# Performance work log

Hardware: AMD Instinct MI355X
Metric: run time of the kernel (lower is better)

Reference implementation:

```python
import jax, jax.numpy as jnp
import numpy as np

B = 16384
INPUT_DIM = 768
DIM = 500
K = 43  # known_types(33) + unknown_types(10)
VAE_DIM = 1024


def setup_inputs() -> dict:
    key = jax.random.key(0)
    ks = jax.random.split(key, 12)
    x = jax.random.normal(ks[0], (B, INPUT_DIM), dtype=jnp.float32)
    known_mask = jax.random.randint(ks[1], (B,), 0, 2) > 0
    labels = jax.random.randint(ks[2], (B,), 0, 33)
    eps = jax.random.normal(ks[3], (B, VAE_DIM), dtype=jnp.float32)
    # encoder MLP (layers_n=1): single Linear(input_dim -> dim)
    W_enc = jax.random.normal(ks[4], (DIM, INPUT_DIM), dtype=jnp.float32) * (1.0 / np.sqrt(INPUT_DIM))
    b_enc = jnp.zeros((DIM,), dtype=jnp.float32)
    # codebook embedding, init U(-1/K, 1/K)
    codebook = jax.random.uniform(ks[5], (K, DIM), dtype=jnp.float32, minval=-1.0 / K, maxval=1.0 / K)
    # vae_encoder MLP (layers_n=2): Linear(input_dim->vae_dim), ReLU, Linear(vae_dim->2*vae_dim)
    W1 = jax.random.normal(ks[6], (VAE_DIM, INPUT_DIM), dtype=jnp.float32) * (1.0 / np.sqrt(INPUT_DIM))
    b1 = jnp.zeros((VAE_DIM,), dtype=jnp.float32)
    W2 = jax.random.normal(ks[7], (2 * VAE_DIM, VAE_DIM), dtype=jnp.float32) * (1.0 / np.sqrt(VAE_DIM))
    b2 = jnp.zeros((2 * VAE_DIM,), dtype=jnp.float32)
    # vae_decoder: Linear(K + vae_dim -> input_dim)
    Wd = jax.random.normal(ks[8], (INPUT_DIM, K + VAE_DIM), dtype=jnp.float32) * (1.0 / np.sqrt(K + VAE_DIM))
    bd = jnp.zeros((INPUT_DIM,), dtype=jnp.float32)
    return {
        "x": x, "known_mask": known_mask, "labels": labels, "eps": eps,
        "W_enc": W_enc, "b_enc": b_enc, "codebook": codebook,
        "W1": W1, "b1": b1, "W2": W2, "b2": b2, "Wd": Wd, "bd": bd,
    }


def reference(x, known_mask, labels, eps, W_enc, b_enc, codebook, W1, b1, W2, b2, Wd, bd):
    # encoder: z_e_x (B, dim)
    z_e_x = x @ W_enc.T + b_enc
    # codebook lookup: logits (B, K); argmax of softmax == argmax of logits
    logits = z_e_x @ codebook.T
    y_tilde = jax.nn.softmax(logits, axis=1)
    indices = jnp.argmax(y_tilde, axis=1)
    z_q_x = codebook[indices]  # (B, dim), differentiable gather w.r.t. codebook
    # VAE encoder: mu, logvar (B, vae_dim)
    h = jax.nn.relu(x @ W1.T + b1)
    mu_logvar = h @ W2.T + b2
    mu, logvar = jnp.split(mu_logvar, 2, axis=1)
    # KL( N(mu, exp(0.5*logvar)) || N(0,1) ), summed over dim, mean over batch
    kl_div = jnp.mean(jnp.sum(0.5 * (jnp.exp(logvar) + mu * mu - 1.0 - logvar), axis=1))
    # reparameterized sample
    sampled_z = mu + jnp.exp(0.5 * logvar) * eps
    # replace known rows of y_tilde with one-hot labels
    onehot = jax.nn.one_hot(labels, logits.shape[1], dtype=y_tilde.dtype)
    y = jnp.where(known_mask[:, None], onehot, y_tilde)
    # vae decoder
    x_tilde = jnp.concatenate([sampled_z, y], axis=1) @ Wd.T + bd
    return (x_tilde, z_e_x, z_q_x, logits, kl_div)
```

## Files before the change

kernel.cpp:

```cpp
#include <hip/hip_runtime.h>
#include <hip/hip_bf16.h>
#include <math.h>


#define B_ROWS 16384

typedef __attribute__((ext_vector_type(8))) short bf16x8;
typedef __attribute__((ext_vector_type(4))) float f32x4;

constexpr size_t X_TILDE_OFF = 0;
constexpr size_t ZE_OFF      = 12582912;
constexpr size_t ZQ_OFF      = 20774912;
constexpr size_t LOG_OFF     = 28966912;
constexpr size_t KL_OFF      = 29671424;

constexpr size_t WS_XH  = 0;
constexpr size_t WS_XL  = 25165824;
constexpr size_t WS_ZB  = 50331648;
constexpr size_t WS_HB  = 85983232;
constexpr size_t WS_MLB = 119537664;
constexpr size_t WS_W1B = 186646528;
constexpr size_t WS_W2B = 188219392;
constexpr size_t WS_WDB = 192413696;
constexpr size_t WS_WEH = 194084864;
constexpr size_t WS_WEL = 194871296;
constexpr size_t WS_CBH = 195657728;
constexpr size_t WS_CBL = 195854336;
constexpr size_t WS_CBD = 196050944;
constexpr size_t WS_LBF = 196315136;
constexpr size_t WS_LBD = 196315648;

__device__ __forceinline__ unsigned short f2b(float f) {
    unsigned u = __builtin_bit_cast(unsigned, f);
    return (unsigned short)((u + 0x7FFFu + ((u >> 16) & 1u)) >> 16);
}
__device__ __forceinline__ float b2f(unsigned short u) {
    return __uint_as_float(((unsigned)u) << 16);
}

__device__ __forceinline__ void stage16(const void* g, void* l) {
    __builtin_amdgcn_global_load_lds(
        (const __attribute__((address_space(1))) void*)g,
        (__attribute__((address_space(3))) void*)l, 16, 0, 0);
}

template<bool RELU, bool OUT_BF16>
__global__ __launch_bounds__(256) void gemm_bf16(
    const unsigned short* __restrict__ A,
    const unsigned short* __restrict__ Bw,
    const float* __restrict__ bias,
    void* __restrict__ Cv,
    int lda, int ldb, int ldc, int K)
{
    __shared__ short As[128 * 32];
    __shared__ short Bs[128 * 32];
    const int t  = threadIdx.x;
    const int w  = t >> 6, l = t & 63;
    const int row0 = blockIdx.y * 128;
    const int col0 = blockIdx.x * 128;
    const int wr = (w >> 1) * 64, wc = (w & 1) * 64;

    const unsigned short* a0 = A  + (size_t)(row0 + (t >> 2)) * lda + ((t & 3) << 3);
    const unsigned short* b0 = Bw + (size_t)(col0 + (t >> 2)) * ldb + ((t & 3) << 3);
    const size_t aStep = (size_t)64 * lda;
    const size_t bStep = (size_t)64 * ldb;
    short* lA0 = As + t * 8;       short* lA1 = As + (256 + t) * 8;
    short* lB0 = Bs + t * 8;       short* lB1 = Bs + (256 + t) * 8;

    f32x4 acc[4][4] = {};
    const int fr = l & 15;
    const int fk = (l >> 4) << 3;

    for (int k0 = 0; k0 < K; k0 += 32) {
        stage16(a0 + k0, lA0);
        stage16(a0 + aStep + k0, lA1);
        stage16(b0 + k0, lB0);
        stage16(b0 + bStep + k0, lB1);
        __syncthreads();
        bf16x8 am[4], bn[4];
        #pragma unroll
        for (int i = 0; i < 4; ++i)
            am[i] = *(const bf16x8*)&As[(wr + i * 16 + fr) * 32 + fk];
        #pragma unroll
        for (int j = 0; j < 4; ++j)
            bn[j] = *(const bf16x8*)&Bs[(wc + j * 16 + fr) * 32 + fk];
        #pragma unroll
        for (int i = 0; i < 4; ++i)
            #pragma unroll
            for (int j = 0; j < 4; ++j)
                acc[i][j] = __builtin_amdgcn_mfma_f32_16x16x32_bf16(
                    am[i], bn[j], acc[i][j], 0, 0, 0);
        __syncthreads();
    }

    const int fq = (l >> 4) << 2;
    #pragma unroll
    for (int i = 0; i < 4; ++i) {
        #pragma unroll
        for (int j = 0; j < 4; ++j) {
            const int c = col0 + wc + j * 16 + fr;
            const int r = row0 + wr + i * 16 + fq;
            const float bv = bias[c];
            #pragma unroll
            for (int q = 0; q < 4; ++q) {
                float v = acc[i][j][q] + bv;
                if (RELU) v = fmaxf(v, 0.f);
                if (OUT_BF16)
                    ((unsigned short*)Cv)[(size_t)(r + q) * ldc + c] = f2b(v);
                else
                    ((float*)Cv)[(size_t)(r + q) * ldc + c] = v;
            }
        }
    }
}

template<bool NGUARD>
__global__ __launch_bounds__(256) void gemm_bf16x3(
    const unsigned short* __restrict__ Ah,
    const unsigned short* __restrict__ Al,
    const unsigned short* __restrict__ Bh,
    const unsigned short* __restrict__ Bl,
    const float* __restrict__ bias,
    float* __restrict__ C,
    int lda, int ldb, int ldc, int N, int K)
{
    __shared__ short sAh[128 * 32];
    __shared__ short sAl[128 * 32];
    __shared__ short sBh[128 * 32];
    __shared__ short sBl[128 * 32];
    const int t  = threadIdx.x;
    const int w  = t >> 6, l = t & 63;
    const int row0 = blockIdx.y * 128;
    const int col0 = blockIdx.x * 128;
    const int wr = (w >> 1) * 64, wc = (w & 1) * 64;

    const size_t aoff  = (size_t)(row0 + (t >> 2)) * lda + ((t & 3) << 3);
    const size_t boff  = (size_t)(col0 + (t >> 2)) * ldb + ((t & 3) << 3);
    const size_t aStep = (size_t)64 * lda;
    const size_t bStep = (size_t)64 * ldb;
    const int l0 = t * 8, l1 = (256 + t) * 8;

    f32x4 acc[4][4] = {};
    const int fr = l & 15;
    const int fk = (l >> 4) << 3;

    for (int k0 = 0; k0 < K; k0 += 32) {
        stage16(Ah + aoff + k0,         sAh + l0);
        stage16(Ah + aoff + aStep + k0, sAh + l1);
        stage16(Al + aoff + k0,         sAl + l0);
        stage16(Al + aoff + aStep + k0, sAl + l1);
        stage16(Bh + boff + k0,         sBh + l0);
        stage16(Bh + boff + bStep + k0, sBh + l1);
        stage16(Bl + boff + k0,         sBl + l0);
        stage16(Bl + boff + bStep + k0, sBl + l1);
        __syncthreads();
        bf16x8 ah[4], al[4], bh[4], bl[4];
        #pragma unroll
        for (int i = 0; i < 4; ++i) {
            ah[i] = *(const bf16x8*)&sAh[(wr + i * 16 + fr) * 32 + fk];
            al[i] = *(const bf16x8*)&sAl[(wr + i * 16 + fr) * 32 + fk];
        }
        #pragma unroll
        for (int j = 0; j < 4; ++j) {
            bh[j] = *(const bf16x8*)&sBh[(wc + j * 16 + fr) * 32 + fk];
            bl[j] = *(const bf16x8*)&sBl[(wc + j * 16 + fr) * 32 + fk];
        }
        #pragma unroll
        for (int i = 0; i < 4; ++i)
            #pragma unroll
            for (int j = 0; j < 4; ++j) {
                acc[i][j] = __builtin_amdgcn_mfma_f32_16x16x32_bf16(
                    ah[i], bh[j], acc[i][j], 0, 0, 0);
                acc[i][j] = __builtin_amdgcn_mfma_f32_16x16x32_bf16(
                    al[i], bh[j], acc[i][j], 0, 0, 0);
                acc[i][j] = __builtin_amdgcn_mfma_f32_16x16x32_bf16(
                    ah[i], bl[j], acc[i][j], 0, 0, 0);
            }
        __syncthreads();
    }

    const int fq = (l >> 4) << 2;
    #pragma unroll
    for (int i = 0; i < 4; ++i) {
        #pragma unroll
        for (int j = 0; j < 4; ++j) {
            const int c = col0 + wc + j * 16 + fr;
            if (!NGUARD || c < N) {
                const int r = row0 + wr + i * 16 + fq;
                const float bv = bias[c];
                #pragma unroll
                for (int q = 0; q < 4; ++q)
                    C[(size_t)(r + q) * ldc + c] = acc[i][j][q] + bv;
            }
        }
    }
}

__global__ __launch_bounds__(256) void cbw_kernel(
    const float* __restrict__ W_enc,
    const float* __restrict__ cb,
    const float* __restrict__ b_enc,
    double* __restrict__ cbWd,
    unsigned short* __restrict__ cbWh,
    unsigned short* __restrict__ cbWl,
    float* __restrict__ lbf,
    double* __restrict__ lbd)
{
    const int j = blockIdx.x;
    const int t = threadIdx.x;
    if (j >= 43) {
        for (int d = t; d < 768; d += 256) {
            cbWh[(size_t)j * 768 + d] = 0;
            cbWl[(size_t)j * 768 + d] = 0;
        }
        if (t == 0) lbf[j] = 0.f;
        return;
    }
    double acc[3] = {0.0, 0.0, 0.0};
    for (int k = 0; k < 500; ++k) {
        const double c = (double)cb[(size_t)j * 500 + k];
        acc[0] = fma(c, (double)W_enc[(size_t)k * 768 + t],       acc[0]);
        acc[1] = fma(c, (double)W_enc[(size_t)k * 768 + t + 256], acc[1]);
        acc[2] = fma(c, (double)W_enc[(size_t)k * 768 + t + 512], acc[2]);
    }
    #pragma unroll
    for (int q = 0; q < 3; ++q) {
        const int d = t + q * 256;
        const double v = acc[q];
        cbWd[(size_t)j * 768 + d] = v;
        const float f = (float)v;
        const unsigned short h = f2b(f);
        cbWh[(size_t)j * 768 + d] = h;
        cbWl[(size_t)j * 768 + d] = f2b(f - b2f(h));
    }
    if (t == 0) {
        double s = 0.0;
        for (int k = 0; k < 500; ++k)
            s = fma((double)cb[(size_t)j * 500 + k], (double)b_enc[k], s);
        lbd[j] = s;
        lbf[j] = (float)s;
    }
}

__global__ __launch_bounds__(256) void head_kernel(
    const float* __restrict__ logits,
    const float* __restrict__ codebook,
    const int* __restrict__ known_mask,
    const int* __restrict__ labels,
    const float* __restrict__ x,
    const double* __restrict__ cbWd,
    const double* __restrict__ lbd,
    float* __restrict__ zq_out,
    unsigned short* __restrict__ Zb)
{
    const int wave = threadIdx.x >> 6;
    const int lane = threadIdx.x & 63;
    const int row  = blockIdx.x * 4 + wave;

    const float* lrow = logits + (size_t)row * 43;
    const float v = (lane < 43) ? lrow[lane] : -INFINITY;

    float bvv = v; int bi = lane;
    #pragma unroll
    for (int off = 32; off; off >>= 1) {
        const float ov = __shfl_xor(bvv, off);
        const int   oi = __shfl_xor(bi, off);
        if (ov > bvv || (ov == bvv && oi < bi)) { bvv = ov; bi = oi; }
    }
    float v2 = (lane == bi) ? -INFINITY : v;
    #pragma unroll
    for (int off = 32; off; off >>= 1) v2 = fmaxf(v2, __shfl_xor(v2, off));

    int idx = bi;
    if (bvv - v2 < 1e-3f) {
        double dv = -1.0e300;
        if (lane < 43) {
            double s = lbd[lane];
            const float* xr = x + (size_t)row * 768;
            const double* wrow = cbWd + (size_t)lane * 768;
            for (int d = 0; d < 768; ++d)
                s = fma((double)xr[d], wrow[d], s);
            dv = s;
        }
        double bdv = dv; int bj = lane;
        #pragma unroll
        for (int off = 32; off; off >>= 1) {
            const double ov = __shfl_xor(bdv, off);
            const int    oi = __shfl_xor(bj, off);
            if (ov > bdv || (ov == bdv && oi < bj)) { bdv = ov; bj = oi; }
        }
        idx = bj;
    }

    float e = (lane < 43) ? expf(v - bvv) : 0.f;
    float s = e;
    #pragma unroll
    for (int off = 32; off; off >>= 1) s += __shfl_xor(s, off);

    const int km  = known_mask[row];
    const int lab = labels[row];
    float y;
    if (lane < 43) y = km ? ((lane == lab) ? 1.f : 0.f) : (e / s);
    else           y = 0.f;
    Zb[(size_t)row * 1088 + 1024 + lane] = f2b(y);

    const float* crow = codebook + (size_t)idx * 500;
    float* zrow = zq_out + (size_t)row * 500;
    for (int c = lane; c < 500; c += 64) zrow[c] = crow[c];
}

__global__ __launch_bounds__(256) void vae_sample(
    const unsigned short* __restrict__ MLb,
    const float* __restrict__ eps,
    unsigned short* __restrict__ Zb,
    float* __restrict__ kl_out)
{
    float klsum = 0.f;
    const int total = B_ROWS * 128;
    for (int g = blockIdx.x * blockDim.x + threadIdx.x; g < total;
         g += gridDim.x * blockDim.x) {
        const int m = g >> 7;
        const int j = (g & 127) << 3;
        const bf16x8 muv = *(const bf16x8*)(MLb + (size_t)m * 2048 + j);
        const bf16x8 lvv = *(const bf16x8*)(MLb + (size_t)m * 2048 + 1024 + j);
        const float4 e0 = *(const float4*)(eps + (size_t)m * 1024 + j);
        const float4 e1 = *(const float4*)(eps + (size_t)m * 1024 + j + 4);
        const float ep[8] = {e0.x, e0.y, e0.z, e0.w, e1.x, e1.y, e1.z, e1.w};
        bf16x8 zv;
        #pragma unroll
        for (int q = 0; q < 8; ++q) {
            const float mu = b2f((unsigned short)muv[q]);
            const float lv = b2f((unsigned short)lvv[q]);
            const float z  = fmaf(expf(0.5f * lv), ep[q], mu);
            zv[q] = (short)f2b(z);
            klsum += 0.5f * (expf(lv) + mu * mu - 1.f - lv);
        }
        *(bf16x8*)(Zb + (size_t)m * 1088 + j) = zv;
    }
    __shared__ float wsum[4];
    const int lane = threadIdx.x & 63, wave = threadIdx.x >> 6;
    #pragma unroll
    for (int off = 32; off; off >>= 1) klsum += __shfl_xor(klsum, off);
    if (lane == 0) wsum[wave] = klsum;
    __syncthreads();
    if (threadIdx.x == 0)
        atomicAdd(kl_out, (wsum[0] + wsum[1] + wsum[2] + wsum[3]) * (1.0f / 16384.f));
}

__global__ __launch_bounds__(256) void conv_split(
    const float* __restrict__ in,
    unsigned short* __restrict__ hi, unsigned short* __restrict__ lo, int n)
{
    const int i = (blockIdx.x * 256 + threadIdx.x) * 4;
    if (i >= n) return;
    const float4 v = *(const float4*)(in + i);
    ushort4 h, l;
    h.x = f2b(v.x); l.x = f2b(v.x - b2f(h.x));
    h.y = f2b(v.y); l.y = f2b(v.y - b2f(h.y));
    h.z = f2b(v.z); l.z = f2b(v.z - b2f(h.z));
    h.w = f2b(v.w); l.w = f2b(v.w - b2f(h.w));
    *(ushort4*)(hi + i) = h;
    *(ushort4*)(lo + i) = l;
}

__global__ __launch_bounds__(256) void wenc_split(
    const float* __restrict__ W,
    unsigned short* __restrict__ hi, unsigned short* __restrict__ lo)
{
    const int idx = blockIdx.x * 256 + threadIdx.x;
    if (idx >= 512 * 768) return;
    const int r = idx / 768;
    if (r < 500) {
        const float v = W[idx];
        const unsigned short h = f2b(v);
        hi[idx] = h;
        lo[idx] = f2b(v - b2f(h));
    } else {
        hi[idx] = 0; lo[idx] = 0;
    }
}

__global__ __launch_bounds__(256) void conv_bf16(
    const float* __restrict__ in, unsigned short* __restrict__ out, int n)
{
    const int i = (blockIdx.x * 256 + threadIdx.x) * 4;
    if (i >= n) return;
    const float4 v = *(const float4*)(in + i);
    ushort4 o;
    o.x = f2b(v.x); o.y = f2b(v.y); o.z = f2b(v.z); o.w = f2b(v.w);
    *(ushort4*)(out + i) = o;
}

__global__ __launch_bounds__(256) void repack_wd(
    const float* __restrict__ Wd, unsigned short* __restrict__ Wdb)
{
    const int idx = blockIdx.x * 256 + threadIdx.x;
    if (idx >= 768 * 1088) return;
    const int n = idx / 1088;
    const int k = idx - n * 1088;
    Wdb[idx] = (k < 1067) ? f2b(Wd[(size_t)n * 1067 + k]) : 0;
}

extern "C" void kernel_launch(void* const* d_in, const int* in_sizes, int n_in,
                              void* d_out, int out_size, void* d_ws, size_t ws_size,
                              hipStream_t stream) {
    const float* x        = (const float*)d_in[0];
    const int*   known    = (const int*)  d_in[1];
    const int*   labels   = (const int*)  d_in[2];
    const float* eps      = (const float*)d_in[3];
    const float* W_enc    = (const float*)d_in[4];
    const float* b_enc    = (const float*)d_in[5];
    const float* codebook = (const float*)d_in[6];
    const float* W1       = (const float*)d_in[7];
    const float* b1       = (const float*)d_in[8];
    const float* W2       = (const float*)d_in[9];
    const float* b2       = (const float*)d_in[10];
    const float* Wd       = (const float*)d_in[11];
    const float* bd       = (const float*)d_in[12];
    float* out = (float*)d_out;
    char*  ws  = (char*)d_ws;

    unsigned short* xh   = (unsigned short*)(ws + WS_XH);
    unsigned short* xl   = (unsigned short*)(ws + WS_XL);
    unsigned short* Zb   = (unsigned short*)(ws + WS_ZB);
    unsigned short* hb   = (unsigned short*)(ws + WS_HB);
    unsigned short* MLb  = (unsigned short*)(ws + WS_MLB);
    unsigned short* W1b  = (unsigned short*)(ws + WS_W1B);
    unsigned short* W2b  = (unsigned short*)(ws + WS_W2B);
    unsigned short* Wdb  = (unsigned short*)(ws + WS_WDB);
    unsigned short* Weh  = (unsigned short*)(ws + WS_WEH);
    unsigned short* Wel  = (unsigned short*)(ws + WS_WEL);
    unsigned short* cbWh = (unsigned short*)(ws + WS_CBH);
    unsigned short* cbWl = (unsigned short*)(ws + WS_CBL);
    double*         cbWd = (double*)        (ws + WS_CBD);
    float*          lbf  = (float*)         (ws + WS_LBF);
    double*         lbd  = (double*)        (ws + WS_LBD);

    hipMemsetAsync(out + KL_OFF, 0, sizeof(float), stream);

    const dim3 blk(256);
    conv_split<<<(16384 * 768 / 4 + 255) / 256, blk, 0, stream>>>(x, xh, xl, 16384 * 768);
    conv_bf16<<<(1024 * 768 / 4 + 255) / 256, blk, 0, stream>>>(W1, W1b, 1024 * 768);
    conv_bf16<<<(2048 * 1024 / 4 + 255) / 256, blk, 0, stream>>>(W2, W2b, 2048 * 1024);
    repack_wd<<<(768 * 1088 + 255) / 256, blk, 0, stream>>>(Wd, Wdb);
    wenc_split<<<(512 * 768 + 255) / 256, blk, 0, stream>>>(W_enc, Weh, Wel);
    cbw_kernel<<<128, blk, 0, stream>>>(W_enc, codebook, b_enc,
                                        cbWd, cbWh, cbWl, lbf, lbd);

    gemm_bf16<true, true><<<dim3(8, B_ROWS / 128), blk, 0, stream>>>(
        xh, W1b, b1, hb, 768, 768, 1024, 768);
    gemm_bf16<false, true><<<dim3(16, B_ROWS / 128), blk, 0, stream>>>(
        hb, W2b, b2, MLb, 1024, 1024, 2048, 1024);
    gemm_bf16x3<true><<<dim3(4, B_ROWS / 128), blk, 0, stream>>>(
        xh, xl, Weh, Wel, b_enc, out + ZE_OFF, 768, 768, 500, 500, 768);
    gemm_bf16x3<true><<<dim3(1, B_ROWS / 128), blk, 0, stream>>>(
        xh, xl, cbWh, cbWl, lbf, out + LOG_OFF, 768, 768, 43, 43, 768);
    head_kernel<<<B_ROWS / 4, blk, 0, stream>>>(
        out + LOG_OFF, codebook, known, labels, x, cbWd, lbd,
        out + ZQ_OFF, Zb);
    vae_sample<<<2048, blk, 0, stream>>>(MLb, eps, Zb, out + KL_OFF);
    gemm_bf16<false, false><<<dim3(6, B_ROWS / 128), blk, 0, stream>>>(
        Zb, Wdb, bd, out + X_TILDE_OFF, 1088, 1088, 768, 1088);
}
```

Before: 642.3 us.

## Double-buffer GEMM loads, fuse VAE sampling into W2 GEMM, drop z_e bf16x3 split

Adds LDS double buffering with async global-to-LDS prefetch to every GEMM, so loads of the next K-slice overlap MFMA work on the current one. The mu/logvar GEMM now uses a W2 repacked to interleave mu and logvar columns, which lets its epilogue compute the reparameterized sample and the KL sum directly. This removes the bf16 mu/logvar intermediate and the separate vae_sample kernel. The z_e_x GEMM switches from three-pass bf16x3 to a single plain bf16 pass, which cuts MFMA work but lowers the precision of that output.

```diff
diff --git a/kernel.cpp b/kernel.cpp
--- a/kernel.cpp
+++ b/kernel.cpp
@@ -18,17 +18,15 @@
 constexpr size_t WS_XL  = 25165824;
 constexpr size_t WS_ZB  = 50331648;
 constexpr size_t WS_HB  = 85983232;
-constexpr size_t WS_MLB = 119537664;
-constexpr size_t WS_W1B = 186646528;
-constexpr size_t WS_W2B = 188219392;
-constexpr size_t WS_WDB = 192413696;
-constexpr size_t WS_WEH = 194084864;
-constexpr size_t WS_WEL = 194871296;
-constexpr size_t WS_CBH = 195657728;
-constexpr size_t WS_CBL = 195854336;
-constexpr size_t WS_CBD = 196050944;
-constexpr size_t WS_LBF = 196315136;
-constexpr size_t WS_LBD = 196315648;
+constexpr size_t WS_W1B = 119537664;
+constexpr size_t WS_W2P = 121110528;
+constexpr size_t WS_WDB = 125304832;
+constexpr size_t WS_WEH = 126976000;
+constexpr size_t WS_CBH = 127762432;
+constexpr size_t WS_CBL = 127959040;
+constexpr size_t WS_CBD = 128155648;
+constexpr size_t WS_LBF = 128419840;
+constexpr size_t WS_LBD = 128420352;
 
 __device__ __forceinline__ unsigned short f2b(float f) {
     unsigned u = __builtin_bit_cast(unsigned, f);
@@ -44,126 +42,181 @@
         (__attribute__((address_space(3))) void*)l, 16, 0, 0);
 }
 
-template<bool RELU, bool OUT_BF16>
-__global__ __launch_bounds__(256) void gemm_bf16(
+__device__ __forceinline__ void gemm_loop(
     const unsigned short* __restrict__ A,
     const unsigned short* __restrict__ Bw,
-    const float* __restrict__ bias,
-    void* __restrict__ Cv,
-    int lda, int ldb, int ldc, int K)
-{
-    __shared__ short As[128 * 32];
-    __shared__ short Bs[128 * 32];
-    const int t  = threadIdx.x;
-    const int w  = t >> 6, l = t & 63;
-    const int row0 = blockIdx.y * 128;
-    const int col0 = blockIdx.x * 128;
+    int lda, int ldb, int K, int row0, int col0,
+    short* As, short* Bs, f32x4 acc[4][4])
+{
+    const int t = threadIdx.x;
+    const int w = t >> 6, l = t & 63;
     const int wr = (w >> 1) * 64, wc = (w & 1) * 64;
-
     const unsigned short* a0 = A  + (size_t)(row0 + (t >> 2)) * lda + ((t & 3) << 3);
     const unsigned short* b0 = Bw + (size_t)(col0 + (t >> 2)) * ldb + ((t & 3) << 3);
-    const size_t aStep = (size_t)64 * lda;
-    const size_t bStep = (size_t)64 * ldb;
-    short* lA0 = As + t * 8;       short* lA1 = As + (256 + t) * 8;
-    short* lB0 = Bs + t * 8;       short* lB1 = Bs + (256 + t) * 8;
-
-    f32x4 acc[4][4] = {};
-    const int fr = l & 15;
-    const int fk = (l >> 4) << 3;
-
+    const size_t aStep = (size_t)64 * lda, bStep = (size_t)64 * ldb;
+    const int fr = l & 15, fk = (l >> 4) << 3;
+    const int s0 = t * 8, s1 = (256 + t) * 8;
+
+    stage16(a0, As + s0); stage16(a0 + aStep, As + s1);
+    stage16(b0, Bs + s0); stage16(b0 + bStep, Bs + s1);
+
+    int cur = 0;
     for (int k0 = 0; k0 < K; k0 += 32) {
-        stage16(a0 + k0, lA0);
-        stage16(a0 + aStep + k0, lA1);
-        stage16(b0 + k0, lB0);
-        stage16(b0 + bStep + k0, lB1);
-        __syncthreads();
+        const int nb = (cur ^ 1) * 4096;
+        if (k0 + 32 < K) {
+            stage16(a0 + k0 + 32,         As + nb + s0);
+            stage16(a0 + aStep + k0 + 32, As + nb + s1);
+            stage16(b0 + k0 + 32,         Bs + nb + s0);
+            stage16(b0 + bStep + k0 + 32, Bs + nb + s1);
+            asm volatile("s_waitcnt vmcnt(4)" ::: "memory");
+        } else {
+            asm volatile("s_waitcnt vmcnt(0)" ::: "memory");
+        }
+        __builtin_amdgcn_s_barrier();
+        const short* cA = As + cur * 4096;
+        const short* cB = Bs + cur * 4096;
         bf16x8 am[4], bn[4];
         #pragma unroll
         for (int i = 0; i < 4; ++i)
-            am[i] = *(const bf16x8*)&As[(wr + i * 16 + fr) * 32 + fk];
+            am[i] = *(const bf16x8*)&cA[(wr + i * 16 + fr) * 32 + fk];
         #pragma unroll
         for (int j = 0; j < 4; ++j)
-            bn[j] = *(const bf16x8*)&Bs[(wc + j * 16 + fr) * 32 + fk];
+            bn[j] = *(const bf16x8*)&cB[(wc + j * 16 + fr) * 32 + fk];
         #pragma unroll
         for (int i = 0; i < 4; ++i)
             #pragma unroll
             for (int j = 0; j < 4; ++j)
                 acc[i][j] = __builtin_amdgcn_mfma_f32_16x16x32_bf16(
                     am[i], bn[j], acc[i][j], 0, 0, 0);
+        __builtin_amdgcn_s_barrier();
+        cur ^= 1;
+    }
+}
+
+enum { EPI_H = 0, EPI_XT = 1, EPI_ZE = 2, EPI_ML = 3 };
+
+template<int EPI>
+__global__ __launch_bounds__(256) void gemm2(
+    const unsigned short* __restrict__ A,
+    const unsigned short* __restrict__ Bw,
+    const float* __restrict__ bias,
+    void* __restrict__ C,
+    const float* __restrict__ eps,
+    float* __restrict__ kl,
+    int lda, int ldb, int ldc, int K)
+{
+    __shared__ short As[2 * 4096];
+    __shared__ short Bs[2 * 4096];
+    __shared__ float wsum[4];
+    f32x4 acc[4][4] = {};
+    const int row0 = blockIdx.y * 128, col0 = blockIdx.x * 128;
+    gemm_loop(A, Bw, lda, ldb, K, row0, col0, As, Bs, acc);
+
+    const int t = threadIdx.x, w = t >> 6, l = t & 63;
+    const int wr = (w >> 1) * 64, wc = (w & 1) * 64;
+    const int fr = l & 15, fq = (l >> 4) << 2;
+
+    if constexpr (EPI == EPI_ML) {
+        float klsum = 0.f;
+        #pragma unroll
+        for (int i = 0; i < 4; ++i) {
+            #pragma unroll
+            for (int jj = 0; jj < 2; ++jj) {
+                const int d = ((col0 + wc) >> 1) + jj * 16 + fr;
+                const float bmu = bias[d], blv = bias[1024 + d];
+                #pragma unroll
+                for (int q = 0; q < 4; ++q) {
+                    const int r = row0 + wr + i * 16 + fq + q;
+                    const float mu = acc[i][2 * jj][q] + bmu;
+                    const float lv = acc[i][2 * jj + 1][q] + blv;
+                    const float e  = eps[(size_t)r * 1024 + d];
+                    const float z  = fmaf(expf(0.5f * lv), e, mu);
+                    ((unsigned short*)C)[(size_t)r * 1088 + d] = f2b(z);
+                    klsum += 0.5f * (expf(lv) + mu * mu - 1.f - lv);
+                }
+            }
+        }
+        #pragma unroll
+        for (int off = 32; off; off >>= 1) klsum += __shfl_xor(klsum, off);
+        if (l == 0) wsum[w] = klsum;
         __syncthreads();
-    }
-
-    const int fq = (l >> 4) << 2;
-    #pragma unroll
-    for (int i = 0; i < 4; ++i) {
-        #pragma unroll
-        for (int j = 0; j < 4; ++j) {
-            const int c = col0 + wc + j * 16 + fr;
-            const int r = row0 + wr + i * 16 + fq;
-            const float bv = bias[c];
+        if (t == 0)
+            atomicAdd(kl, (wsum[0] + wsum[1] + wsum[2] + wsum[3]) * (1.0f / 16384.f));
+    } else {
+        #pragma unroll
+        for (int i = 0; i < 4; ++i) {
             #pragma unroll
-            for (int q = 0; q < 4; ++q) {
-                float v = acc[i][j][q] + bv;
-                if (RELU) v = fmaxf(v, 0.f);
-                if (OUT_BF16)
-                    ((unsigned short*)Cv)[(size_t)(r + q) * ldc + c] = f2b(v);
-                else
-                    ((float*)Cv)[(size_t)(r + q) * ldc + c] = v;
+            for (int j = 0; j < 4; ++j) {
+                const int c = col0 + wc + j * 16 + fr;
+                if (EPI == EPI_ZE && c >= 500) continue;
+                const int r0 = row0 + wr + i * 16 + fq;
+                const float bv = bias[c];
+                #pragma unroll
+                for (int q = 0; q < 4; ++q) {
+                    float v = acc[i][j][q] + bv;
+                    if (EPI == EPI_H) v = fmaxf(v, 0.f);
+                    if (EPI == EPI_H)
+                        ((unsigned short*)C)[(size_t)(r0 + q) * ldc + c] = f2b(v);
+                    else
+                        ((float*)C)[(size_t)(r0 + q) * ldc + c] = v;
+                }
             }
         }
     }
 }
 
-template<bool NGUARD>
-__global__ __launch_bounds__(256) void gemm_bf16x3(
+__global__ __launch_bounds__(256) void gemm_x3_logits(
     const unsigned short* __restrict__ Ah,
     const unsigned short* __restrict__ Al,
     const unsigned short* __restrict__ Bh,
     const unsigned short* __restrict__ Bl,
     const float* __restrict__ bias,
-    float* __restrict__ C,
-    int lda, int ldb, int ldc, int N, int K)
-{
-    __shared__ short sAh[128 * 32];
-    __shared__ short sAl[128 * 32];
-    __shared__ short sBh[128 * 32];
-    __shared__ short sBl[128 * 32];
-    const int t  = threadIdx.x;
-    const int w  = t >> 6, l = t & 63;
+    float* __restrict__ C, int K)
+{
+    __shared__ short sAh[2 * 4096], sAl[2 * 4096];
+    __shared__ short sBh[2 * 4096], sBl[2 * 4096];
+    const int t = threadIdx.x, w = t >> 6, l = t & 63;
     const int row0 = blockIdx.y * 128;
-    const int col0 = blockIdx.x * 128;
     const int wr = (w >> 1) * 64, wc = (w & 1) * 64;
-
-    const size_t aoff  = (size_t)(row0 + (t >> 2)) * lda + ((t & 3) << 3);
-    const size_t boff  = (size_t)(col0 + (t >> 2)) * ldb + ((t & 3) << 3);
-    const size_t aStep = (size_t)64 * lda;
-    const size_t bStep = (size_t)64 * ldb;
-    const int l0 = t * 8, l1 = (256 + t) * 8;
-
+    const size_t aoff = (size_t)(row0 + (t >> 2)) * 768 + ((t & 3) << 3);
+    const size_t boff = (size_t)(t >> 2) * 768 + ((t & 3) << 3);
+    const size_t step = (size_t)64 * 768;
+    const int s0 = t * 8, s1 = (256 + t) * 8;
+    const int fr = l & 15, fk = (l >> 4) << 3;
     f32x4 acc[4][4] = {};
-    const int fr = l & 15;
-    const int fk = (l >> 4) << 3;
-
+
+    #define STAGE_ALL(buf, k)                                                  \
+        stage16(Ah + aoff + (k),        sAh + (buf) * 4096 + s0);              \
+        stage16(Ah + aoff + step + (k), sAh + (buf) * 4096 + s1);              \
+        stage16(Al + aoff + (k),        sAl + (buf) * 4096 + s0);              \
+        stage16(Al + aoff + step + (k), sAl + (buf) * 4096 + s1);              \
+        stage16(Bh + boff + (k),        sBh + (buf) * 4096 + s0);              \
+        stage16(Bh + boff + step + (k), sBh + (buf) * 4096 + s1);              \
+        stage16(Bl + boff + (k),        sBl + (buf) * 4096 + s0);              \
+        stage16(Bl + boff + step + (k), sBl + (buf) * 4096 + s1);
+
+    STAGE_ALL(0, 0)
+    int cur = 0;
     for (int k0 = 0; k0 < K; k0 += 32) {
-        stage16(Ah + aoff + k0,         sAh + l0);
-        stage16(Ah + aoff + aStep + k0, sAh + l1);
-        stage16(Al + aoff + k0,         sAl + l0);
-        stage16(Al + aoff + aStep + k0, sAl + l1);
-        stage16(Bh + boff + k0,         sBh + l0);
-        stage16(Bh + boff + bStep + k0, sBh + l1);
-        stage16(Bl + boff + k0,         sBl + l0);
-        stage16(Bl + boff + bStep + k0, sBl + l1);
-        __syncthreads();
+        if (k0 + 32 < K) {
+            STAGE_ALL(cur ^ 1, k0 + 32)
+            asm volatile("s_waitcnt vmcnt(8)" ::: "memory");
+        } else {
+            asm volatile("s_waitcnt vmcnt(0)" ::: "memory");
+        }
+        __builtin_amdgcn_s_barrier();
+        const short* cAh = sAh + cur * 4096;  const short* cAl = sAl + cur * 4096;
+        const short* cBh = sBh + cur * 4096;  const short* cBl = sBl + cur * 4096;
         bf16x8 ah[4], al[4], bh[4], bl[4];
         #pragma unroll
         for (int i = 0; i < 4; ++i) {
-            ah[i] = *(const bf16x8*)&sAh[(wr + i * 16 + fr) * 32 + fk];
-            al[i] = *(const bf16x8*)&sAl[(wr + i * 16 + fr) * 32 + fk];
+            ah[i] = *(const bf16x8*)&cAh[(wr + i * 16 + fr) * 32 + fk];
+            al[i] = *(const bf16x8*)&cAl[(wr + i * 16 + fr) * 32 + fk];
         }
         #pragma unroll
         for (int j = 0; j < 4; ++j) {
-            bh[j] = *(const bf16x8*)&sBh[(wc + j * 16 + fr) * 32 + fk];
-            bl[j] = *(const bf16x8*)&sBl[(wc + j * 16 + fr) * 32 + fk];
+            bh[j] = *(const bf16x8*)&cBh[(wc + j * 16 + fr) * 32 + fk];
+            bl[j] = *(const bf16x8*)&cBl[(wc + j * 16 + fr) * 32 + fk];
         }
         #pragma unroll
         for (int i = 0; i < 4; ++i)
@@ -176,34 +229,32 @@
                 acc[i][j] = __builtin_amdgcn_mfma_f32_16x16x32_bf16(
                     ah[i], bl[j], acc[i][j], 0, 0, 0);
             }
-        __syncthreads();
-    }
+        __builtin_amdgcn_s_barrier();
+        cur ^= 1;
+    }
+    #undef STAGE_ALL
 
     const int fq = (l >> 4) << 2;
     #pragma unroll
-    for (int i = 0; i < 4; ++i) {
+    for (int i = 0; i < 4; ++i)
         #pragma unroll
         for (int j = 0; j < 4; ++j) {
-            const int c = col0 + wc + j * 16 + fr;
-            if (!NGUARD || c < N) {
-                const int r = row0 + wr + i * 16 + fq;
+            const int c = wc + j * 16 + fr;
+            if (c < 43) {
+                const int r0 = row0 + wr + i * 16 + fq;
                 const float bv = bias[c];
                 #pragma unroll
                 for (int q = 0; q < 4; ++q)
-                    C[(size_t)(r + q) * ldc + c] = acc[i][j][q] + bv;
+                    C[(size_t)(r0 + q) * 43 + c] = acc[i][j][q] + bv;
             }
         }
-    }
 }
 
 __global__ __launch_bounds__(256) void cbw_kernel(
-    const float* __restrict__ W_enc,
-    const float* __restrict__ cb,
+    const float* __restrict__ W_enc, const float* __restrict__ cb,
     const float* __restrict__ b_enc,
-    double* __restrict__ cbWd,
-    unsigned short* __restrict__ cbWh,
-    unsigned short* __restrict__ cbWl,
-    float* __restrict__ lbf,
+    double* __restrict__ cbWd, unsigned short* __restrict__ cbWh,
+    unsigned short* __restrict__ cbWl, float* __restrict__ lbf,
     double* __restrict__ lbd)
 {
     const int j = blockIdx.x;
@@ -243,15 +294,11 @@
 }
 
 __global__ __launch_bounds__(256) void head_kernel(
-    const float* __restrict__ logits,
-    const float* __restrict__ codebook,
-    const int* __restrict__ known_mask,
-    const int* __restrict__ labels,
-    const float* __restrict__ x,
-    const double* __restrict__ cbWd,
+    const float* __restrict__ logits, const float* __restrict__ codebook,
+    const int* __restrict__ known_mask, const int* __restrict__ labels,
+    const float* __restrict__ x, const double* __restrict__ cbWd,
     const double* __restrict__ lbd,
-    float* __restrict__ zq_out,
-    unsigned short* __restrict__ Zb)
+    float* __restrict__ zq_out, unsigned short* __restrict__ Zb)
 {
     const int wave = threadIdx.x >> 6;
     const int lane = threadIdx.x & 63;
@@ -309,44 +356,6 @@
     for (int c = lane; c < 500; c += 64) zrow[c] = crow[c];
 }
 
-__global__ __launch_bounds__(256) void vae_sample(
-    const unsigned short* __restrict__ MLb,
-    const float* __restrict__ eps,
-    unsigned short* __restrict__ Zb,
-    float* __restrict__ kl_out)
-{
-    float klsum = 0.f;
-    const int total = B_ROWS * 128;
-    for (int g = blockIdx.x * blockDim.x + threadIdx.x; g < total;
-         g += gridDim.x * blockDim.x) {
-        const int m = g >> 7;
-        const int j = (g & 127) << 3;
-        const bf16x8 muv = *(const bf16x8*)(MLb + (size_t)m * 2048 + j);
-        const bf16x8 lvv = *(const bf16x8*)(MLb + (size_t)m * 2048 + 1024 + j);
-        const float4 e0 = *(const float4*)(eps + (size_t)m * 1024 + j);
-        const float4 e1 = *(const float4*)(eps + (size_t)m * 1024 + j + 4);
-        const float ep[8] = {e0.x, e0.y, e0.z, e0.w, e1.x, e1.y, e1.z, e1.w};
-        bf16x8 zv;
-        #pragma unroll
-        for (int q = 0; q < 8; ++q) {
-            const float mu = b2f((unsigned short)muv[q]);
-            const float lv = b2f((unsigned short)lvv[q]);
-            const float z  = fmaf(expf(0.5f * lv), ep[q], mu);
-            zv[q] = (short)f2b(z);
-            klsum += 0.5f * (expf(lv) + mu * mu - 1.f - lv);
-        }
-        *(bf16x8*)(Zb + (size_t)m * 1088 + j) = zv;
-    }
-    __shared__ float wsum[4];
-    const int lane = threadIdx.x & 63, wave = threadIdx.x >> 6;
-    #pragma unroll
-    for (int off = 32; off; off >>= 1) klsum += __shfl_xor(klsum, off);
-    if (lane == 0) wsum[wave] = klsum;
-    __syncthreads();
-    if (threadIdx.x == 0)
-        atomicAdd(kl_out, (wsum[0] + wsum[1] + wsum[2] + wsum[3]) * (1.0f / 16384.f));
-}
-
 __global__ __launch_bounds__(256) void conv_split(
     const float* __restrict__ in,
     unsigned short* __restrict__ hi, unsigned short* __restrict__ lo, int n)
@@ -363,23 +372,6 @@
     *(ushort4*)(lo + i) = l;
 }
 
-__global__ __launch_bounds__(256) void wenc_split(
-    const float* __restrict__ W,
-    unsigned short* __restrict__ hi, unsigned short* __restrict__ lo)
-{
-    const int idx = blockIdx.x * 256 + threadIdx.x;
-    if (idx >= 512 * 768) return;
-    const int r = idx / 768;
-    if (r < 500) {
-        const float v = W[idx];
-        const unsigned short h = f2b(v);
-        hi[idx] = h;
-        lo[idx] = f2b(v - b2f(h));
-    } else {
-        hi[idx] = 0; lo[idx] = 0;
-    }
-}
-
 __global__ __launch_bounds__(256) void conv_bf16(
     const float* __restrict__ in, unsigned short* __restrict__ out, int n)
 {
@@ -389,6 +381,27 @@
     ushort4 o;
     o.x = f2b(v.x); o.y = f2b(v.y); o.z = f2b(v.z); o.w = f2b(v.w);
     *(ushort4*)(out + i) = o;
+}
+
+__global__ __launch_bounds__(256) void wenc_hi(
+    const float* __restrict__ W, unsigned short* __restrict__ hi)
+{
+    const int idx = blockIdx.x * 256 + threadIdx.x;
+    if (idx >= 512 * 768) return;
+    const int r = idx / 768;
+    hi[idx] = (r < 500) ? f2b(W[idx]) : 0;
+}
+
+__global__ __launch_bounds__(256) void repack_w2p(
+    const float* __restrict__ W2, unsigned short* __restrict__ W2p)
+{
+    const int idx = blockIdx.x * 256 + threadIdx.x;
+    if (idx >= 2048 * 1024) return;
+    const int c = idx >> 10;
+    const int k = idx & 1023;
+    const int s = c & 31, g = c >> 5;
+    const int src = ((s < 16) ? 0 : 1024) + g * 16 + (s & 15);
+    W2p[idx] = f2b(W2[(size_t)src * 1024 + k]);
 }
 
 __global__ __launch_bounds__(256) void repack_wd(
@@ -424,12 +437,10 @@
     unsigned short* xl   = (unsigned short*)(ws + WS_XL);
     unsigned short* Zb   = (unsigned short*)(ws + WS_ZB);
     unsigned short* hb   = (unsigned short*)(ws + WS_HB);
-    unsigned short* MLb  = (unsigned short*)(ws + WS_MLB);
     unsigned short* W1b  = (unsigned short*)(ws + WS_W1B);
-    unsigned short* W2b  = (unsigned short*)(ws + WS_W2B);
+    unsigned short* W2p  = (unsigned short*)(ws + WS_W2P);
     unsigned short* Wdb  = (unsigned short*)(ws + WS_WDB);
     unsigned short* Weh  = (unsigned short*)(ws + WS_WEH);
-    unsigned short* Wel  = (unsigned short*)(ws + WS_WEL);
     unsigned short* cbWh = (unsigned short*)(ws + WS_CBH);
     unsigned short* cbWl = (unsigned short*)(ws + WS_CBL);
     double*         cbWd = (double*)        (ws + WS_CBD);
@@ -441,24 +452,23 @@
     const dim3 blk(256);
     conv_split<<<(16384 * 768 / 4 + 255) / 256, blk, 0, stream>>>(x, xh, xl, 16384 * 768);
     conv_bf16<<<(1024 * 768 / 4 + 255) / 256, blk, 0, stream>>>(W1, W1b, 1024 * 768);
-    conv_bf16<<<(2048 * 1024 / 4 + 255) / 256, blk, 0, stream>>>(W2, W2b, 2048 * 1024);
+    repack_w2p<<<(2048 * 1024 + 255) / 256, blk, 0, stream>>>(W2, W2p);
     repack_wd<<<(768 * 1088 + 255) / 256, blk, 0, stream>>>(Wd, Wdb);
-    wenc_split<<<(512 * 768 + 255) / 256, blk, 0, stream>>>(W_enc, Weh, Wel);
+    wenc_hi<<<(512 * 768 + 255) / 256, blk, 0, stream>>>(W_enc, Weh);
     cbw_kernel<<<128, blk, 0, stream>>>(W_enc, codebook, b_enc,
                                         cbWd, cbWh, cbWl, lbf, lbd);
 
-    gemm_bf16<true, true><<<dim3(8, B_ROWS / 128), blk, 0, stream>>>(
-        xh, W1b, b1, hb, 768, 768, 1024, 768);
-    gemm_bf16<false, true><<<dim3(16, B_ROWS / 128), blk, 0, stream>>>(
-        hb, W2b, b2, MLb, 1024, 1024, 2048, 1024);
-    gemm_bf16x3<true><<<dim3(4, B_ROWS / 128), blk, 0, stream>>>(
-        xh, xl, Weh, Wel, b_enc, out + ZE_OFF, 768, 768, 500, 500, 768);
-    gemm_bf16x3<true><<<dim3(1, B_ROWS / 128), blk, 0, stream>>>(
-        xh, xl, cbWh, cbWl, lbf, out + LOG_OFF, 768, 768, 43, 43, 768);
+    gemm2<EPI_H><<<dim3(8, 128), blk, 0, stream>>>(
+        xh, W1b, b1, hb, nullptr, nullptr, 768, 768, 1024, 768);
+    gemm2<EPI_ML><<<dim3(16, 128), blk, 0, stream>>>(
+        hb, W2p, b2, Zb, eps, out + KL_OFF, 1024, 1024, 0, 1024);
+    gemm2<EPI_ZE><<<dim3(4, 128), blk, 0, stream>>>(
+        xh, Weh, b_enc, out + ZE_OFF, nullptr, nullptr, 768, 768, 500, 768);
+    gemm_x3_logits<<<dim3(1, 128), blk, 0, stream>>>(
+        xh, xl, cbWh, cbWl, lbf, out + LOG_OFF, 768);
     head_kernel<<<B_ROWS / 4, blk, 0, stream>>>(
         out + LOG_OFF, codebook, known, labels, x, cbWd, lbd,
         out + ZQ_OFF, Zb);
-    vae_sample<<<2048, blk, 0, stream>>>(MLb, eps, Zb, out + KL_OFF);
-    gemm_bf16<false, false><<<dim3(6, B_ROWS / 128), blk, 0, stream>>>(
-        Zb, Wdb, bd, out + X_TILDE_OFF, 1088, 1088, 768, 1088);
-}
+    gemm2<EPI_XT><<<dim3(6, 128), blk, 0, stream>>>(
+        Zb, Wdb, bd, out + X_TILDE_OFF, nullptr, nullptr, 1088, 1088, 768, 1088);
+}
```

Result: faster. 593.8 us (-7.6%).
